# Kernel tuning notes

Hardware: AMD Instinct MI355X
Metric: run time of the kernel (lower is better)

The kernel has to match this reference:

```python
import jax, jax.numpy as jnp
import numpy as np

N = 1048576
HID = 256
GEO = 15
POS_LAT = 3 + 10 * 2 * 3  # 63
DIR_LAT = 3 + 4 * 2 * 3   # 27
AABB_MIN = -1.5
AABB_MAX = 1.5


def sinus_enc(x, min_deg, max_deg):
    # x: [..., 3] -> [..., 3 + (max_deg-min_deg)*2*3] (identity + sin/cos bands)
    scales = 2.0 ** jnp.arange(min_deg, max_deg, dtype=x.dtype)
    xb = (x[..., None, :] * scales[:, None]).reshape(
        x.shape[:-1] + ((max_deg - min_deg) * x.shape[-1],))
    latent = jnp.sin(jnp.concatenate([xb, xb + 0.5 * np.pi], axis=-1))
    return jnp.concatenate([x, latent], axis=-1)


def trunc_exp(x):
    return jnp.exp(x)


def setup_inputs() -> dict:
    key = jax.random.key(0)
    ks = jax.random.split(key, 12)
    positions = jax.random.uniform(ks[0], (N, 3), dtype=jnp.float32,
                                   minval=AABB_MIN, maxval=AABB_MAX)
    directions = jax.random.normal(ks[1], (N, 3), dtype=jnp.float32)
    s = 0.05
    return {
        "positions": positions,
        "directions": directions,
        "W1": jax.random.normal(ks[2], (POS_LAT, HID), jnp.float32) * s,
        "b1": jnp.zeros((HID,), jnp.float32),
        "W2": jax.random.normal(ks[3], (HID, HID), jnp.float32) * s,
        "b2": jnp.zeros((HID,), jnp.float32),
        "W3": jax.random.normal(ks[4], (HID, HID), jnp.float32) * s,
        "b3": jnp.zeros((HID,), jnp.float32),
        "W4": jax.random.normal(ks[5], (HID, 1 + GEO), jnp.float32) * s,
        "b4": jnp.zeros((1 + GEO,), jnp.float32),
        "Wc1": jax.random.normal(ks[6], (GEO + DIR_LAT, HID // 2), jnp.float32) * s,
        "bc1": jnp.zeros((HID // 2,), jnp.float32),
        "Wc2": jax.random.normal(ks[7], (HID // 2, 3), jnp.float32) * s,
        "bc2": jnp.zeros((3,), jnp.float32),
    }


def reference(positions, directions, W1, b1, W2, b2, W3, b3, W4, b4,
              Wc1, bc1, Wc2, bc2):
    # normalize positions into [-1, 1] within the aabb
    x = (positions - AABB_MIN) / (AABB_MAX - AABB_MIN) * 2.0 - 1.0
    pe = sinus_enc(x, 0, 10)  # [N, 63]
    h = jax.nn.relu(pe @ W1 + b1)
    h = jax.nn.relu(h @ W2 + b2)
    h = jax.nn.relu(h @ W3 + b3)
    h = h @ W4 + b4  # [N, 16]
    density = trunc_exp(h[..., 0:1] - 1.0)  # [N, 1]
    feat = h[..., 1:]  # [N, 15]

    nrm = jnp.linalg.norm(directions, axis=-1, keepdims=True)
    d = directions / jnp.maximum(nrm, 1e-12)
    de = sinus_enc(d, 0, 4)  # [N, 27]
    hc = jnp.concatenate([feat, de], axis=-1)  # [N, 42]
    hc = jax.nn.relu(hc @ Wc1 + bc1)
    rgb = jax.nn.sigmoid(hc @ Wc2 + bc2)  # [N, 3]
    return rgb, density
```

## Files before the change

kernel.cpp:

```cpp
#include <hip/hip_runtime.h>

typedef unsigned short u16;
typedef __attribute__((ext_vector_type(8))) short short8;
typedef __attribute__((ext_vector_type(4))) float f32x4;
typedef __attribute__((ext_vector_type(16))) float f32x16;
typedef __attribute__((ext_vector_type(2))) unsigned int u32x2;

#define NPTS 1048576
#define TILES 128
#define NBLK (NPTS / (32 * TILES))
#define HPE 72
#define HPB 264
#define HPF 136

__device__ __forceinline__ u16 f2b(float f) {
    return (u16)((__float_as_uint(f) + 0x8000u) >> 16);
}
#define INV2PI 0.15915494309189535f
__device__ __forceinline__ float sinrev(float t) {
    t = t - floorf(t);
    return __builtin_amdgcn_sinf(t);
}

__global__ void prep_weights(const float* __restrict__ W1, const float* __restrict__ b1,
                             const float* __restrict__ W2,
                             const float* __restrict__ W3, const float* __restrict__ W4,
                             const float* __restrict__ Wc1, const float* __restrict__ bc1,
                             const float* __restrict__ Wc2,
                             u16* __restrict__ ws) {
    int i = blockIdx.x * 256 + threadIdx.x;
    if (i < 16384) { int n = i >> 6, k = i & 63;  ws[i]          = (k < 63) ? f2b(W1[k * 256 + n]) : f2b(b1[n]); return; }
    i -= 16384;
    if (i < 65536) { int n = i >> 8, k = i & 255; ws[16384 + i]  = f2b(W2[k * 256 + n]); return; }
    i -= 65536;
    if (i < 65536) { int n = i >> 8, k = i & 255; ws[81920 + i]  = f2b(W3[k * 256 + n]); return; }
    i -= 65536;
    if (i < 4096)  { int n = i >> 8, k = i & 255; ws[147456 + i] = f2b(W4[k * 16 + n]); return; }
    i -= 4096;
    if (i < 8192)  { int n = i >> 6, k = i & 63;
                     ws[151552 + i] = (k < 42) ? f2b(Wc1[k * 128 + n]) : ((k == 42) ? f2b(bc1[n]) : (u16)0); return; }
    i -= 8192;
    if (i < 2048)  { int n = i >> 7, k = i & 127; ws[159744 + i] = (n < 3) ? f2b(Wc2[k * 3 + n]) : (u16)0; return; }
}

template <bool BIAS>
__device__ __forceinline__ void epi32(const f32x16& acc, u16* rowp, const float* bias,
                                      int nbase, int kh) {
#pragma unroll
    for (int g = 0; g < 4; ++g) {
        const int mq = nbase + 8 * g + 4 * kh;
        float v[4];
#pragma unroll
        for (int j = 0; j < 4; ++j) v[j] = acc[4 * g + j];
        if (BIAS) {
            const f32x4 bi = *(const f32x4*)(bias + mq);
#pragma unroll
            for (int j = 0; j < 4; ++j) v[j] += bi[j];
        }
#pragma unroll
        for (int j = 0; j < 4; ++j) v[j] = fmaxf(v[j], 0.f);
        unsigned int u[4];
#pragma unroll
        for (int j = 0; j < 4; ++j) u[j] = __float_as_uint(v[j]) + 0x8000u;
        u32x2 d;
        d.x = __builtin_amdgcn_perm(u[1], u[0], 0x07060302);
        d.y = __builtin_amdgcn_perm(u[3], u[2], 0x07060302);
        *(u32x2*)(rowp + mq) = d;
    }
}

template <int NKT, bool BIAS>
__device__ __forceinline__ void layer32(const short8* wr, const u16* src, int ss,
                                        u16* dst, int ds, const float* bias,
                                        int nbase, int ln, int kh) {
    f32x16 acc;
#pragma unroll
    for (int r = 0; r < 16; ++r) acc[r] = 0.f;
#pragma unroll
    for (int kt = 0; kt < NKT; ++kt) {
        const short8 bA = *(const short8*)(src + ln * ss + kt * 16 + kh * 8);
        acc = __builtin_amdgcn_mfma_f32_32x32x16_bf16(wr[kt], bA, acc, 0, 0, 0);
    }
    epi32<BIAS>(acc, dst + ln * ds, bias, nbase, kh);
}

__device__ __forceinline__ void enc_preload(const float* __restrict__ pos,
                                            const float* __restrict__ dir,
                                            long rb, int t, float* v) {
    if (t < 256) {
        const long row = rb + (t >> 3);
        v[0] = pos[row * 3 + 0]; v[1] = pos[row * 3 + 1]; v[2] = pos[row * 3 + 2];
    } else {
        const long row = rb + ((t - 256) >> 3);
        v[0] = dir[row * 3 + 0]; v[1] = dir[row * 3 + 1]; v[2] = dir[row * 3 + 2];
    }
}

__device__ __forceinline__ void enc_compute(const float* v, int t, u16* sEj, u16* sGj) {
    if (t < 256) {
        const int r = t >> 3, g = t & 7;
        float xn[3];
#pragma unroll
        for (int c = 0; c < 3; ++c) xn[c] = v[c] * (1.0f / 1.5f);
        u16* er = sEj + r * HPE;
        if (g < 5) {
#pragma unroll
            for (int dd = 0; dd < 2; ++dd) {
                const int d = 2 * g + dd;
                const float sc = (float)(1 << d);
#pragma unroll
                for (int c = 0; c < 3; ++c) {
                    float tv = xn[c] * sc * INV2PI;
                    er[3 + d * 3 + c]  = f2b(sinrev(tv));
                    er[33 + d * 3 + c] = f2b(sinrev(tv + 0.25f));
                }
            }
        } else if (g == 5) {
            er[0] = f2b(xn[0]); er[1] = f2b(xn[1]); er[2] = f2b(xn[2]);
            er[63] = 0x3F80;
        }
    } else {
        const int t2 = t - 256;
        const int r = t2 >> 3, g = t2 & 7;
        u16* gr = sGj + r * HPE;
        const float dx = v[0], dy = v[1], dz = v[2];
        if (g < 6) {
            const float nrm = sqrtf(dx * dx + dy * dy + dz * dz);
            const float inv = 1.f / fmaxf(nrm, 1e-12f);
            const float dn[3] = {dx * inv, dy * inv, dz * inv};
            if (g < 4) {
                const float sc = (float)(1 << g);
#pragma unroll
                for (int c = 0; c < 3; ++c) {
                    float tv = dn[c] * sc * INV2PI;
                    gr[18 + g * 3 + c] = f2b(sinrev(tv));
                    gr[30 + g * 3 + c] = f2b(sinrev(tv + 0.25f));
                }
            } else if (g == 4) {
                gr[15] = f2b(dn[0]); gr[16] = f2b(dn[1]); gr[17] = f2b(dn[2]);
            } else {
                gr[42] = 0x3F80;
#pragma unroll
                for (int c = 43; c < 50; ++c) gr[c] = 0;
            }
        } else if (g == 6) {
#pragma unroll
            for (int c = 50; c < 57; ++c) gr[c] = 0;
        } else {
#pragma unroll
            for (int c = 57; c < 64; ++c) gr[c] = 0;
        }
    }
}

__global__ __launch_bounds__(1024, 4) void ngp_fused(
    const float* __restrict__ pos, const float* __restrict__ dir, const u16* __restrict__ ws,
    const float* __restrict__ b2, const float* __restrict__ b3,
    const float* __restrict__ b4, const float* __restrict__ bc2,
    float* __restrict__ out) {
    __shared__ __align__(16) u16 sE[2][32][HPE];
    __shared__ __align__(16) u16 sB[32][HPB];
    __shared__ __align__(16) u16 sC[32][HPB];
    __shared__ __align__(16) u16 sD[32][HPB];
    __shared__ __align__(16) u16 sG[4][32][HPE];
    __shared__ __align__(16) u16 sF[2][32][HPF];
    const int t = threadIdx.x;
    const int lane = t & 63;
    const int w = t >> 6;
    const int bw = w - 8;
    const int ln = lane & 31, kh = lane >> 5;
    const int lr = lane & 15, q = lane >> 4;

    const u16* WT1  = ws;
    const u16* WT2  = ws + 16384;
    const u16* WT3  = ws + 81920;
    const u16* WT4  = ws + 147456;
    const u16* WTc1 = ws + 151552;
    const u16* WTc2 = ws + 159744;

    short8 wrA[16], wrB[4];
    {
        const u16* pA = (w < 8) ? WT2 + (size_t)(w * 32 + ln) * 256 + kh * 8
                                : WT3 + (size_t)(bw * 32 + ln) * 256 + kh * 8;
#pragma unroll
        for (int kt = 0; kt < 16; ++kt) wrA[kt] = *(const short8*)(pA + kt * 16);
        const u16* pB = (w < 8)  ? WT1 + (size_t)(w * 32 + ln) * 64 + kh * 8
                      : (bw < 4) ? WTc1 + (size_t)(bw * 32 + ln) * 64 + kh * 8
                                 : WT1 + (size_t)ln * 64 + kh * 8;
#pragma unroll
        for (int kt = 0; kt < 4; ++kt) wrB[kt] = *(const short8*)(pB + kt * 16);
    }

    {
        float pv[3];
        if (t < 512) {
            enc_preload(pos, dir, (long)blockIdx.x * TILES * 32, t, pv);
            enc_compute(pv, t, &sE[0][0][0], &sG[0][0][0]);
        }
        __syncthreads();
    }

    for (int i = 0; i <= TILES + 2; ++i) {
        const bool dL1  = (i < TILES);
        const bool dEnc = (i + 1 < TILES);
        const bool dL3  = (i >= 1 && i <= TILES);
        const bool dC1  = (i >= 2 && i <= TILES + 1);
        const bool dHd  = (i >= 3);

        float pv[3];
        if (dEnc && t < 512)
            enc_preload(pos, dir, ((long)blockIdx.x * TILES + i + 1) * 32, t, pv);
        if (dL1 && w < 8)
            layer32<4, false>(wrB, &sE[i & 1][0][0], HPE, &sB[0][0], HPB, nullptr, w * 32, ln, kh);
        if (dL3 && w >= 8)
            layer32<16, true>(wrA, &sC[0][0], HPB, &sD[0][0], HPB, b3, bw * 32, ln, kh);
        if (dEnc && t < 512)
            enc_compute(pv, t, &sE[(i + 1) & 1][0][0], &sG[(i + 1) & 3][0][0]);
        __syncthreads();

        if (dL1 && w < 8)
            layer32<16, true>(wrA, &sB[0][0], HPB, &sC[0][0], HPB, b2, w * 32, ln, kh);
        if (dL3 && w >= 8 && (bw == 4 || bw == 5)) {
            const long rbM = ((long)blockIdx.x * TILES + i - 1) * 32;
            u16* sGf = &sG[(i - 1) & 3][0][0];
            const int rbase = (bw - 4) * 16;
            f32x4 acc = {0.f, 0.f, 0.f, 0.f};
#pragma unroll
            for (int kt = 0; kt < 8; ++kt) {
                const short8 aF = *(const short8*)&sD[rbase + lr][kt * 32 + q * 8];
                const short8 bF = *(const short8*)(WT4 + lr * 256 + kt * 32 + q * 8);
                acc = __builtin_amdgcn_mfma_f32_16x16x32_bf16(aF, bF, acc, 0, 0, 0);
            }
            const float bi = b4[lr];
#pragma unroll
            for (int r = 0; r < 4; ++r) {
                const float v = acc[r] + bi;
                const int gm = rbase + q * 4 + r;
                if (lr == 0)
                    out[3 * (long)NPTS + rbM + gm] = __expf(v - 1.f);
                else
                    sGf[gm * HPE + lr - 1] = f2b(v);
            }
        }
        if (dC1 && w >= 8 && bw < 4)
            layer32<4, false>(wrB, &sG[(i - 2) & 3][0][0], HPE, &sF[(i - 2) & 1][0][0], HPF,
                              nullptr, bw * 32, ln, kh);
        if (dHd && w >= 8 && (bw == 6 || bw == 7)) {
            const long rbH = ((long)blockIdx.x * TILES + i - 3) * 32;
            const int rbase = (bw - 6) * 16;
            f32x4 acc = {0.f, 0.f, 0.f, 0.f};
#pragma unroll
            for (int kt = 0; kt < 4; ++kt) {
                const short8 aF = *(const short8*)&sF[(i - 3) & 1][rbase + lr][kt * 32 + q * 8];
                const short8 bF = *(const short8*)(WTc2 + lr * 128 + kt * 32 + q * 8);
                acc = __builtin_amdgcn_mfma_f32_16x16x32_bf16(aF, bF, acc, 0, 0, 0);
            }
            if (lr < 3) {
                const float bi = bc2[lr];
#pragma unroll
                for (int r = 0; r < 4; ++r) {
                    const float v = acc[r] + bi;
                    const float sg = 1.f / (1.f + __expf(-v));
                    out[(rbH + rbase + q * 4 + r) * 3 + lr] = sg;
                }
            }
        }
        __syncthreads();
    }
}

extern "C" void kernel_launch(void* const* d_in, const int* in_sizes, int n_in,
                              void* d_out, int out_size, void* d_ws, size_t ws_size,
                              hipStream_t stream) {
    const float* pos = (const float*)d_in[0];
    const float* dir = (const float*)d_in[1];
    const float* W1  = (const float*)d_in[2];
    const float* b1  = (const float*)d_in[3];
    const float* W2  = (const float*)d_in[4];
    const float* b2  = (const float*)d_in[5];
    const float* W3  = (const float*)d_in[6];
    const float* b3  = (const float*)d_in[7];
    const float* W4  = (const float*)d_in[8];
    const float* b4  = (const float*)d_in[9];
    const float* Wc1 = (const float*)d_in[10];
    const float* bc1 = (const float*)d_in[11];
    const float* Wc2 = (const float*)d_in[12];
    const float* bc2 = (const float*)d_in[13];
    u16* ws   = (u16*)d_ws;
    float* out = (float*)d_out;

    prep_weights<<<633, 256, 0, stream>>>(W1, b1, W2, W3, W4, Wc1, bc1, Wc2, ws);
    ngp_fused<<<NBLK, 1024, 0, stream>>>(pos, dir, ws, b2, b3, b4, bc2, out);
}
```

Before: 562.4 us.

## Deepen cross-tile pipeline to one barrier per iteration with double-buffered activations

Each block's loop goes from two barriers per tile to one. The activation buffers sB, sC and sD become double-buffered and the geometry-feature ring grows from 4 to 6 slots, so the stages (L1, L2, L3, L4, C1, head) each work on a different tile in the same phase. The front eight waves now run layers 1 and 2, and the back eight waves run the input encoding plus layer 3, the density/feature head and the colour layers. This is meant to cut barrier stalls and balance MFMA work between the two wave groups. The cost is much more LDS per block (close to the per-CU limit) and two more pipeline fill/drain iterations.

```diff
diff --git a/kernel.cpp b/kernel.cpp
--- a/kernel.cpp
+++ b/kernel.cpp
@@ -86,19 +86,19 @@
 
 __device__ __forceinline__ void enc_preload(const float* __restrict__ pos,
                                             const float* __restrict__ dir,
-                                            long rb, int t, float* v) {
-    if (t < 256) {
-        const long row = rb + (t >> 3);
+                                            long rb, int j, float* v) {
+    if (j < 256) {
+        const long row = rb + (j >> 3);
         v[0] = pos[row * 3 + 0]; v[1] = pos[row * 3 + 1]; v[2] = pos[row * 3 + 2];
     } else {
-        const long row = rb + ((t - 256) >> 3);
+        const long row = rb + ((j - 256) >> 3);
         v[0] = dir[row * 3 + 0]; v[1] = dir[row * 3 + 1]; v[2] = dir[row * 3 + 2];
     }
 }
 
-__device__ __forceinline__ void enc_compute(const float* v, int t, u16* sEj, u16* sGj) {
-    if (t < 256) {
-        const int r = t >> 3, g = t & 7;
+__device__ __forceinline__ void enc_compute(const float* v, int j, u16* sEj, u16* sGj) {
+    if (j < 256) {
+        const int r = j >> 3, g = j & 7;
         float xn[3];
 #pragma unroll
         for (int c = 0; c < 3; ++c) xn[c] = v[c] * (1.0f / 1.5f);
@@ -120,8 +120,8 @@
             er[63] = 0x3F80;
         }
     } else {
-        const int t2 = t - 256;
-        const int r = t2 >> 3, g = t2 & 7;
+        const int j2 = j - 256;
+        const int r = j2 >> 3, g = j2 & 7;
         u16* gr = sGj + r * HPE;
         const float dx = v[0], dy = v[1], dz = v[2];
         if (g < 6) {
@@ -159,10 +159,10 @@
     const float* __restrict__ b4, const float* __restrict__ bc2,
     float* __restrict__ out) {
     __shared__ __align__(16) u16 sE[2][32][HPE];
-    __shared__ __align__(16) u16 sB[32][HPB];
-    __shared__ __align__(16) u16 sC[32][HPB];
-    __shared__ __align__(16) u16 sD[32][HPB];
-    __shared__ __align__(16) u16 sG[4][32][HPE];
+    __shared__ __align__(16) u16 sB[2][32][HPB];
+    __shared__ __align__(16) u16 sC[2][32][HPB];
+    __shared__ __align__(16) u16 sD[2][32][HPB];
+    __shared__ __align__(16) u16 sG[6][32][HPE];
     __shared__ __align__(16) u16 sF[2][32][HPF];
     const int t = threadIdx.x;
     const int lane = t & 63;
@@ -193,79 +193,89 @@
 
     {
         float pv[3];
-        if (t < 512) {
-            enc_preload(pos, dir, (long)blockIdx.x * TILES * 32, t, pv);
-            enc_compute(pv, t, &sE[0][0][0], &sG[0][0][0]);
+        if (t >= 512) {
+            enc_preload(pos, dir, (long)blockIdx.x * TILES * 32, t - 512, pv);
+            enc_compute(pv, t - 512, &sE[0][0][0], &sG[0][0][0]);
         }
         __syncthreads();
     }
 
-    for (int i = 0; i <= TILES + 2; ++i) {
+    int gE = 1;
+    for (int i = 0; i <= TILES + 4; ++i) {
+        const bool dEnc = (i + 1 < TILES);
         const bool dL1  = (i < TILES);
-        const bool dEnc = (i + 1 < TILES);
-        const bool dL3  = (i >= 1 && i <= TILES);
-        const bool dC1  = (i >= 2 && i <= TILES + 1);
-        const bool dHd  = (i >= 3);
-
-        float pv[3];
-        if (dEnc && t < 512)
-            enc_preload(pos, dir, ((long)blockIdx.x * TILES + i + 1) * 32, t, pv);
-        if (dL1 && w < 8)
-            layer32<4, false>(wrB, &sE[i & 1][0][0], HPE, &sB[0][0], HPB, nullptr, w * 32, ln, kh);
-        if (dL3 && w >= 8)
-            layer32<16, true>(wrA, &sC[0][0], HPB, &sD[0][0], HPB, b3, bw * 32, ln, kh);
-        if (dEnc && t < 512)
-            enc_compute(pv, t, &sE[(i + 1) & 1][0][0], &sG[(i + 1) & 3][0][0]);
-        __syncthreads();
-
-        if (dL1 && w < 8)
-            layer32<16, true>(wrA, &sB[0][0], HPB, &sC[0][0], HPB, b2, w * 32, ln, kh);
-        if (dL3 && w >= 8 && (bw == 4 || bw == 5)) {
-            const long rbM = ((long)blockIdx.x * TILES + i - 1) * 32;
-            u16* sGf = &sG[(i - 1) & 3][0][0];
-            const int rbase = (bw - 4) * 16;
-            f32x4 acc = {0.f, 0.f, 0.f, 0.f};
-#pragma unroll
-            for (int kt = 0; kt < 8; ++kt) {
-                const short8 aF = *(const short8*)&sD[rbase + lr][kt * 32 + q * 8];
-                const short8 bF = *(const short8*)(WT4 + lr * 256 + kt * 32 + q * 8);
-                acc = __builtin_amdgcn_mfma_f32_16x16x32_bf16(aF, bF, acc, 0, 0, 0);
-            }
-            const float bi = b4[lr];
-#pragma unroll
-            for (int r = 0; r < 4; ++r) {
-                const float v = acc[r] + bi;
-                const int gm = rbase + q * 4 + r;
-                if (lr == 0)
-                    out[3 * (long)NPTS + rbM + gm] = __expf(v - 1.f);
-                else
-                    sGf[gm * HPE + lr - 1] = f2b(v);
-            }
-        }
-        if (dC1 && w >= 8 && bw < 4)
-            layer32<4, false>(wrB, &sG[(i - 2) & 3][0][0], HPE, &sF[(i - 2) & 1][0][0], HPF,
-                              nullptr, bw * 32, ln, kh);
-        if (dHd && w >= 8 && (bw == 6 || bw == 7)) {
-            const long rbH = ((long)blockIdx.x * TILES + i - 3) * 32;
-            const int rbase = (bw - 6) * 16;
-            f32x4 acc = {0.f, 0.f, 0.f, 0.f};
-#pragma unroll
-            for (int kt = 0; kt < 4; ++kt) {
-                const short8 aF = *(const short8*)&sF[(i - 3) & 1][rbase + lr][kt * 32 + q * 8];
-                const short8 bF = *(const short8*)(WTc2 + lr * 128 + kt * 32 + q * 8);
-                acc = __builtin_amdgcn_mfma_f32_16x16x32_bf16(aF, bF, acc, 0, 0, 0);
-            }
-            if (lr < 3) {
-                const float bi = bc2[lr];
+        const bool dL2  = (i >= 1 && i <= TILES);
+        const bool dL3  = (i >= 2 && i <= TILES + 1);
+        const bool dL4  = (i >= 3 && i <= TILES + 2);
+        const bool dC1  = (i >= 4 && i <= TILES + 3);
+        const bool dHd  = (i >= 5);
+        int gF = gE + 2; if (gF >= 6) gF -= 6;
+        int gC = gE + 1; if (gC >= 6) gC -= 6;
+
+        if (w < 8) {
+            if (dL2)
+                layer32<16, true>(wrA, &sB[(i - 1) & 1][0][0], HPB, &sC[(i - 1) & 1][0][0], HPB,
+                                  b2, w * 32, ln, kh);
+            if (dL1)
+                layer32<4, false>(wrB, &sE[i & 1][0][0], HPE, &sB[i & 1][0][0], HPB,
+                                  nullptr, w * 32, ln, kh);
+        } else {
+            float pv[3];
+            if (dEnc)
+                enc_preload(pos, dir, ((long)blockIdx.x * TILES + i + 1) * 32, t - 512, pv);
+            if (dL3)
+                layer32<16, true>(wrA, &sC[(i - 2) & 1][0][0], HPB, &sD[(i - 2) & 1][0][0], HPB,
+                                  b3, bw * 32, ln, kh);
+            if (dL4 && (bw == 4 || bw == 5)) {
+                const long rbM = ((long)blockIdx.x * TILES + i - 3) * 32;
+                u16* sGf = &sG[gF][0][0];
+                const int rbase = (bw - 4) * 16;
+                f32x4 acc = {0.f, 0.f, 0.f, 0.f};
+#pragma unroll
+                for (int kt = 0; kt < 8; ++kt) {
+                    const short8 aF = *(const short8*)&sD[(i - 3) & 1][rbase + lr][kt * 32 + q * 8];
+                    const short8 bF = *(const short8*)(WT4 + lr * 256 + kt * 32 + q * 8);
+                    acc = __builtin_amdgcn_mfma_f32_16x16x32_bf16(aF, bF, acc, 0, 0, 0);
+                }
+                const float bi = b4[lr];
 #pragma unroll
                 for (int r = 0; r < 4; ++r) {
                     const float v = acc[r] + bi;
-                    const float sg = 1.f / (1.f + __expf(-v));
-                    out[(rbH + rbase + q * 4 + r) * 3 + lr] = sg;
+                    const int gm = rbase + q * 4 + r;
+                    if (lr == 0)
+                        out[3 * (long)NPTS + rbM + gm] = __expf(v - 1.f);
+                    else
+                        sGf[gm * HPE + lr - 1] = f2b(v);
                 }
             }
+            if (dC1 && bw < 4)
+                layer32<4, false>(wrB, &sG[gC][0][0], HPE, &sF[(i - 4) & 1][0][0], HPF,
+                                  nullptr, bw * 32, ln, kh);
+            if (dHd && (bw == 6 || bw == 7)) {
+                const long rbH = ((long)blockIdx.x * TILES + i - 5) * 32;
+                const int rbase = (bw - 6) * 16;
+                f32x4 acc = {0.f, 0.f, 0.f, 0.f};
+#pragma unroll
+                for (int kt = 0; kt < 4; ++kt) {
+                    const short8 aF = *(const short8*)&sF[(i - 5) & 1][rbase + lr][kt * 32 + q * 8];
+                    const short8 bF = *(const short8*)(WTc2 + lr * 128 + kt * 32 + q * 8);
+                    acc = __builtin_amdgcn_mfma_f32_16x16x32_bf16(aF, bF, acc, 0, 0, 0);
+                }
+                if (lr < 3) {
+                    const float bi = bc2[lr];
+#pragma unroll
+                    for (int r = 0; r < 4; ++r) {
+                        const float v = acc[r] + bi;
+                        const float sg = 1.f / (1.f + __expf(-v));
+                        out[(rbH + rbase + q * 4 + r) * 3 + lr] = sg;
+                    }
+                }
+            }
+            if (dEnc)
+                enc_compute(pv, t - 512, &sE[(i + 1) & 1][0][0], &sG[gE][0][0]);
         }
         __syncthreads();
+        gE = (gE + 1 == 6) ? 0 : gE + 1;
     }
 }
 
```

Result: slower. 594.8 us (+5.7%).

## Rebalance encoding work across waves and raise priority around MFMA loops

Applied to the files above, without the earlier changes.

The sinusoidal encoding is redistributed so each of the first eight waves handles four rows with 16 lanes per row. Each lane loads both position and direction and computes up to four encoding entries. This replaces the old scheme, where threads 0-255 did positions and 256-511 did directions with uneven per-thread work. s_setprio is also raised around the MFMA loops so matrix waves are favoured in issue arbitration over encoding and epilogue work. The change trades duplicate pos/dir loads across 16 lanes, plus more branchy index math, for better load balance and less divergence.

```diff
diff --git a/kernel.cpp b/kernel.cpp
--- a/kernel.cpp
+++ b/kernel.cpp
@@ -76,79 +76,70 @@
     f32x16 acc;
 #pragma unroll
     for (int r = 0; r < 16; ++r) acc[r] = 0.f;
+    __builtin_amdgcn_s_setprio(1);
 #pragma unroll
     for (int kt = 0; kt < NKT; ++kt) {
         const short8 bA = *(const short8*)(src + ln * ss + kt * 16 + kh * 8);
         acc = __builtin_amdgcn_mfma_f32_32x32x16_bf16(wr[kt], bA, acc, 0, 0, 0);
     }
+    __builtin_amdgcn_s_setprio(0);
     epi32<BIAS>(acc, dst + ln * ds, bias, nbase, kh);
 }
 
-__device__ __forceinline__ void enc_preload(const float* __restrict__ pos,
-                                            const float* __restrict__ dir,
-                                            long rb, int t, float* v) {
-    if (t < 256) {
-        const long row = rb + (t >> 3);
-        v[0] = pos[row * 3 + 0]; v[1] = pos[row * 3 + 1]; v[2] = pos[row * 3 + 2];
-    } else {
-        const long row = rb + ((t - 256) >> 3);
-        v[0] = dir[row * 3 + 0]; v[1] = dir[row * 3 + 1]; v[2] = dir[row * 3 + 2];
-    }
-}
-
-__device__ __forceinline__ void enc_compute(const float* v, int t, u16* sEj, u16* sGj) {
-    if (t < 256) {
-        const int r = t >> 3, g = t & 7;
-        float xn[3];
-#pragma unroll
-        for (int c = 0; c < 3; ++c) xn[c] = v[c] * (1.0f / 1.5f);
-        u16* er = sEj + r * HPE;
-        if (g < 5) {
-#pragma unroll
-            for (int dd = 0; dd < 2; ++dd) {
-                const int d = 2 * g + dd;
-                const float sc = (float)(1 << d);
-#pragma unroll
-                for (int c = 0; c < 3; ++c) {
-                    float tv = xn[c] * sc * INV2PI;
-                    er[3 + d * 3 + c]  = f2b(sinrev(tv));
-                    er[33 + d * 3 + c] = f2b(sinrev(tv + 0.25f));
-                }
-            }
-        } else if (g == 5) {
-            er[0] = f2b(xn[0]); er[1] = f2b(xn[1]); er[2] = f2b(xn[2]);
+__device__ __forceinline__ void enc_loads(const float* __restrict__ pos,
+                                          const float* __restrict__ dir,
+                                          long rb, int w, int lane, float* v) {
+    const long row = rb + w * 4 + (lane >> 4);
+    v[0] = pos[row * 3 + 0]; v[1] = pos[row * 3 + 1]; v[2] = pos[row * 3 + 2];
+    v[3] = dir[row * 3 + 0]; v[4] = dir[row * 3 + 1]; v[5] = dir[row * 3 + 2];
+}
+
+__device__ __forceinline__ void enc_compute(const float* v, int w, int lane,
+                                            u16* sEj, u16* sGj) {
+    const int rl = w * 4 + (lane >> 4);
+    const int j16 = lane & 15;
+    u16* er = sEj + rl * HPE;
+    u16* gr = sGj + rl * HPE;
+    const float xn0 = v[0] * (1.0f / 1.5f);
+    const float xn1 = v[1] * (1.0f / 1.5f);
+    const float xn2 = v[2] * (1.0f / 1.5f);
+#pragma unroll
+    for (int k = 0; k < 4; ++k) {
+        const int task = j16 + 16 * k;
+        if (task < 60) {
+            const int ph = (task >= 30) ? 1 : 0;
+            const int m = task - 30 * ph;
+            const int d = m / 3, c = m - 3 * d;
+            const float xv = (c == 0) ? xn0 : ((c == 1) ? xn1 : xn2);
+            const float tv = xv * (float)(1 << d) * INV2PI + (ph ? 0.25f : 0.0f);
+            er[3 + d * 3 + c + 30 * ph] = f2b(sinrev(tv));
+        } else if (task < 63) {
+            const int c = task - 60;
+            er[c] = f2b((c == 0) ? xn0 : ((c == 1) ? xn1 : xn2));
+        } else {
             er[63] = 0x3F80;
         }
-    } else {
-        const int t2 = t - 256;
-        const int r = t2 >> 3, g = t2 & 7;
-        u16* gr = sGj + r * HPE;
-        const float dx = v[0], dy = v[1], dz = v[2];
-        if (g < 6) {
-            const float nrm = sqrtf(dx * dx + dy * dy + dz * dz);
-            const float inv = 1.f / fmaxf(nrm, 1e-12f);
-            const float dn[3] = {dx * inv, dy * inv, dz * inv};
-            if (g < 4) {
-                const float sc = (float)(1 << g);
-#pragma unroll
-                for (int c = 0; c < 3; ++c) {
-                    float tv = dn[c] * sc * INV2PI;
-                    gr[18 + g * 3 + c] = f2b(sinrev(tv));
-                    gr[30 + g * 3 + c] = f2b(sinrev(tv + 0.25f));
-                }
-            } else if (g == 4) {
-                gr[15] = f2b(dn[0]); gr[16] = f2b(dn[1]); gr[17] = f2b(dn[2]);
-            } else {
-                gr[42] = 0x3F80;
-#pragma unroll
-                for (int c = 43; c < 50; ++c) gr[c] = 0;
-            }
-        } else if (g == 6) {
-#pragma unroll
-            for (int c = 50; c < 57; ++c) gr[c] = 0;
-        } else {
-#pragma unroll
-            for (int c = 57; c < 64; ++c) gr[c] = 0;
+    }
+    const float nrm = sqrtf(v[3] * v[3] + v[4] * v[4] + v[5] * v[5]);
+    const float inv = 1.f / fmaxf(nrm, 1e-12f);
+    const float dn0 = v[3] * inv, dn1 = v[4] * inv, dn2 = v[5] * inv;
+#pragma unroll
+    for (int k = 0; k < 4; ++k) {
+        const int task = j16 + 16 * k;
+        if (task < 24) {
+            const int ph = (task >= 12) ? 1 : 0;
+            const int m = task - 12 * ph;
+            const int d = m / 3, c = m - 3 * d;
+            const float dv = (c == 0) ? dn0 : ((c == 1) ? dn1 : dn2);
+            const float tv = dv * (float)(1 << d) * INV2PI + (ph ? 0.25f : 0.0f);
+            gr[18 + d * 3 + c + 12 * ph] = f2b(sinrev(tv));
+        } else if (task < 27) {
+            const int c = task - 24;
+            gr[15 + c] = f2b((c == 0) ? dn0 : ((c == 1) ? dn1 : dn2));
+        } else if (task == 27) {
+            gr[42] = 0x3F80;
+        } else if (task < 49) {
+            gr[task + 15] = 0;
         }
     }
 }
@@ -192,45 +183,48 @@
     }
 
     {
-        float pv[3];
-        if (t < 512) {
-            enc_preload(pos, dir, (long)blockIdx.x * TILES * 32, t, pv);
-            enc_compute(pv, t, &sE[0][0][0], &sG[0][0][0]);
+        float pv[6];
+        if (w < 8) {
+            enc_loads(pos, dir, (long)blockIdx.x * TILES * 32, w, lane, pv);
+            enc_compute(pv, w, lane, &sE[0][0][0], &sG[0][0][0]);
         }
         __syncthreads();
     }
 
     for (int i = 0; i <= TILES + 2; ++i) {
+        const bool dEnc = (i + 1 < TILES);
         const bool dL1  = (i < TILES);
-        const bool dEnc = (i + 1 < TILES);
         const bool dL3  = (i >= 1 && i <= TILES);
+        const bool dL4  = (i >= 1 && i <= TILES);
         const bool dC1  = (i >= 2 && i <= TILES + 1);
         const bool dHd  = (i >= 3);
 
-        float pv[3];
-        if (dEnc && t < 512)
-            enc_preload(pos, dir, ((long)blockIdx.x * TILES + i + 1) * 32, t, pv);
+        float pv[6];
+        if (dEnc && w < 8)
+            enc_loads(pos, dir, ((long)blockIdx.x * TILES + i + 1) * 32, w, lane, pv);
         if (dL1 && w < 8)
             layer32<4, false>(wrB, &sE[i & 1][0][0], HPE, &sB[0][0], HPB, nullptr, w * 32, ln, kh);
         if (dL3 && w >= 8)
             layer32<16, true>(wrA, &sC[0][0], HPB, &sD[0][0], HPB, b3, bw * 32, ln, kh);
-        if (dEnc && t < 512)
-            enc_compute(pv, t, &sE[(i + 1) & 1][0][0], &sG[(i + 1) & 3][0][0]);
+        if (dEnc && w < 8)
+            enc_compute(pv, w, lane, &sE[(i + 1) & 1][0][0], &sG[(i + 1) & 3][0][0]);
         __syncthreads();
 
         if (dL1 && w < 8)
             layer32<16, true>(wrA, &sB[0][0], HPB, &sC[0][0], HPB, b2, w * 32, ln, kh);
-        if (dL3 && w >= 8 && (bw == 4 || bw == 5)) {
+        if (dL4 && w >= 8 && (bw == 4 || bw == 5)) {
             const long rbM = ((long)blockIdx.x * TILES + i - 1) * 32;
             u16* sGf = &sG[(i - 1) & 3][0][0];
             const int rbase = (bw - 4) * 16;
             f32x4 acc = {0.f, 0.f, 0.f, 0.f};
+            __builtin_amdgcn_s_setprio(1);
 #pragma unroll
             for (int kt = 0; kt < 8; ++kt) {
                 const short8 aF = *(const short8*)&sD[rbase + lr][kt * 32 + q * 8];
                 const short8 bF = *(const short8*)(WT4 + lr * 256 + kt * 32 + q * 8);
                 acc = __builtin_amdgcn_mfma_f32_16x16x32_bf16(aF, bF, acc, 0, 0, 0);
             }
+            __builtin_amdgcn_s_setprio(0);
             const float bi = b4[lr];
 #pragma unroll
             for (int r = 0; r < 4; ++r) {
@@ -249,12 +243,14 @@
             const long rbH = ((long)blockIdx.x * TILES + i - 3) * 32;
             const int rbase = (bw - 6) * 16;
             f32x4 acc = {0.f, 0.f, 0.f, 0.f};
+            __builtin_amdgcn_s_setprio(1);
 #pragma unroll
             for (int kt = 0; kt < 4; ++kt) {
                 const short8 aF = *(const short8*)&sF[(i - 3) & 1][rbase + lr][kt * 32 + q * 8];
                 const short8 bF = *(const short8*)(WTc2 + lr * 128 + kt * 32 + q * 8);
                 acc = __builtin_amdgcn_mfma_f32_16x16x32_bf16(aF, bF, acc, 0, 0, 0);
             }
+            __builtin_amdgcn_s_setprio(0);
             if (lr < 3) {
                 const float bi = bc2[lr];
 #pragma unroll
```

Measured after the change: 803.1 us. 1.43x slower.
